# Kernel optimization log

Measured on AMD Instinct MI355X. Metric: run time of the kernel, lower is better.

## Reference

```python
import jax, jax.numpy as jnp
import numpy as np

EPS_NORM = 1e-10
EPS_EXP = 1e-6


def setup_inputs() -> dict:
    key = jax.random.key(0)
    k1, k2 = jax.random.split(key)
    B, F, H, W = 16, 2048, 8, 8
    X = jax.random.normal(k1, (B, F, H, W), dtype=jnp.float32)
    M = jax.random.normal(k2, (B, F, H, W), dtype=jnp.float32)
    return {"X": X, "M": M}


def reference(X, M):
    B, F, H, W = X.shape
    N = H * W
    X = X.reshape(B, F, N)
    M = M.reshape(B, F, N)

    # feature centering over dim=-2 (the feature axis of (B, F, N))
    X = X - X.mean(axis=1, keepdims=True)
    M = M - M.mean(axis=1, keepdims=True)

    # feature_normalize: L2 norm over dim 1, keepdim, + eps
    X = X / (jnp.linalg.norm(X, axis=1, keepdims=True) + EPS_NORM)
    M = M / (jnp.linalg.norm(M, axis=1, keepdims=True) + EPS_NORM)

    # MatmulTopkLoss: S = X @ M^T over spatial N -> (B, F, F)
    S = jnp.einsum('bfn,bgn->bfg', X, M)
    YX = S + jnp.transpose(S, (0, 2, 1))  # symmetrize
    P = jax.nn.softmax(YX, axis=-1)

    k = F // 2
    value, idx = jax.lax.top_k(P, k)  # (B, F, k) values desc, indices
    value_sum = value.sum(axis=-1, keepdims=True)
    row_pos = jnp.arange(F)[None, :, None]  # (1, F, 1)
    dist = jnp.abs(idx - row_pos).astype(value.dtype)
    C_xy = (value * dist / value_sum).mean(axis=-1)  # (B, F)

    xy = jnp.exp(-C_xy + C_xy.min() - EPS_EXP)
    return jnp.reshape(xy.mean(), (1,))
```

## Files before the change

### kernel.cpp

```cpp
#include <hip/hip_runtime.h>
#include <hip/hip_bf16.h>
#include <math.h>

#define B_   16
#define F_   2048
#define N_   64
#define K_   1024
#define YP   2056

typedef short bf16x8 __attribute__((ext_vector_type(8)));
typedef float v4f    __attribute__((ext_vector_type(4)));

__device__ __forceinline__ float wave_sum(float v) {
#pragma unroll
  for (int off = 32; off > 0; off >>= 1) v += __shfl_down(v, off, 64);
  return v;
}
__device__ __forceinline__ float wave_max(float v) {
#pragma unroll
  for (int off = 32; off > 0; off >>= 1) v = fmaxf(v, __shfl_down(v, off, 64));
  return v;
}

__device__ __forceinline__ unsigned f2bf(float x) {
  const unsigned u = __float_as_uint(x);
  return (u + 0x7FFFu + ((u >> 16) & 1u)) >> 16;
}
__device__ __forceinline__ float bf2f(unsigned us) {
  return __uint_as_float(us << 16);
}
__device__ __forceinline__ unsigned ord2u16(unsigned T) {
  return (T & 0x8000u) ? (T ^ 0x8000u) : (T ^ 0xFFFFu);
}

__global__ __launch_bounds__(256) void stats_kernel(
    const float* __restrict__ X, const float* __restrict__ M,
    float* __restrict__ gstats) {
  const int tid = threadIdx.x;
  const int b = blockIdx.x >> 4;
  const int f0 = (blockIdx.x & 15) * 128;
  const int fi = tid >> 6, n = tid & 63;
  float sx = 0.f, sxx = 0.f, sm = 0.f, smm = 0.f;
#pragma unroll 4
  for (int j = 0; j < 32; ++j) {
    const int f = f0 + fi + 4 * j;
    const size_t gi = ((size_t)b * F_ + f) * N_ + n;
    const float x = X[gi];
    const float m = M[gi];
    sx += x; sxx += x * x; sm += m; smm += m * m;
  }
  float* g = gstats + ((size_t)b * N_ + n) * 4;
  atomicAdd(&g[0], sx);
  atomicAdd(&g[1], sxx);
  atomicAdd(&g[2], sm);
  atomicAdd(&g[3], smm);
}

__global__ __launch_bounds__(256) void normbf_kernel(
    const float* __restrict__ X, const float* __restrict__ M,
    const float* __restrict__ gstats,
    short* __restrict__ Xb16, short* __restrict__ Mb16) {
  const int tid = threadIdx.x;
  const int b = blockIdx.x >> 4;
  const int f0 = (blockIdx.x & 15) * 128;
  const int n = tid & 63;
  const float* g = gstats + ((size_t)b * N_ + n) * 4;
  const float sx = g[0], sxx = g[1], sm = g[2], smm = g[3];
  const float mux = sx * (1.f / F_), mum = sm * (1.f / F_);
  const float rx = 1.f / (sqrtf(fmaxf(sxx - (float)F_ * mux * mux, 0.f)) + 1e-10f);
  const float rm = 1.f / (sqrtf(fmaxf(smm - (float)F_ * mum * mum, 0.f)) + 1e-10f);
#pragma unroll 4
  for (int jj = 0; jj < 32; ++jj) {
    const int f = f0 + (tid >> 6) + 4 * jj;
    const size_t gi = ((size_t)b * F_ + f) * N_ + n;
    Xb16[gi] = (short)f2bf((X[gi] - mux) * rx);
    Mb16[gi] = (short)f2bf((M[gi] - mum) * rm);
  }
}

__global__ __launch_bounds__(512)
__attribute__((amdgpu_waves_per_eu(4, 4)))
void rows_kernel(
    const short* __restrict__ Xb16, const short* __restrict__ Mb16,
    float* __restrict__ C) {
  __shared__ unsigned short yxu[16 * YP];
  __shared__ unsigned histS[8 * 256];

  const int tid = threadIdx.x;
  const int w = tid >> 6, lane = tid & 63;
  const int nl = lane & 15, q = lane >> 4;
  const int b = blockIdx.x >> 7;
  const int f0 = (blockIdx.x & 127) * 16;
  const int g0 = 256 * w;

  const short* __restrict__ Xb = Xb16 + (size_t)b * F_ * N_;
  const short* __restrict__ Mb = Mb16 + (size_t)b * F_ * N_;

  const short* Ax = Xb + (size_t)(f0 + nl) * N_ + 8 * q;
  const short* Am = Mb + (size_t)(f0 + nl) * N_ + 8 * q;
  const bf16x8 ax0 = *(const bf16x8*)(Ax);
  const bf16x8 ax1 = *(const bf16x8*)(Ax + 32);
  const bf16x8 am0 = *(const bf16x8*)(Am);
  const bf16x8 am1 = *(const bf16x8*)(Am + 32);

  v4f acc[16];
#pragma unroll
  for (int t = 0; t < 16; ++t) acc[t] = (v4f)(0.f);

#pragma unroll
  for (int t = 0; t < 16; ++t) {
    const short* Bm = Mb + (size_t)(g0 + 16 * t + nl) * N_ + 8 * q;
    const short* Bx = Xb + (size_t)(g0 + 16 * t + nl) * N_ + 8 * q;
    const bf16x8 bm0 = *(const bf16x8*)(Bm);
    const bf16x8 bm1 = *(const bf16x8*)(Bm + 32);
    const bf16x8 bx0 = *(const bf16x8*)(Bx);
    const bf16x8 bx1 = *(const bf16x8*)(Bx + 32);
    acc[t] = __builtin_amdgcn_mfma_f32_16x16x32_bf16(ax0, bm0, acc[t], 0, 0, 0);
    acc[t] = __builtin_amdgcn_mfma_f32_16x16x32_bf16(ax1, bm1, acc[t], 0, 0, 0);
    acc[t] = __builtin_amdgcn_mfma_f32_16x16x32_bf16(am0, bx0, acc[t], 0, 0, 0);
    acc[t] = __builtin_amdgcn_mfma_f32_16x16x32_bf16(am1, bx1, acc[t], 0, 0, 0);
  }

#pragma unroll
  for (int t = 0; t < 16; ++t) {
    const int col = g0 + 16 * t + nl;
#pragma unroll
    for (int r = 0; r < 4; ++r)
      yxu[(4 * q + r) * YP + col] = (unsigned short)f2bf(acc[t][r]);
  }
  __syncthreads();

  unsigned* wh = &histS[w << 8];
#pragma unroll 1
  for (int r4 = 0; r4 < 2; ++r4) {
    const int row = 2 * w + r4;
    const int frow = f0 + row;
    const uint4* rp = (const uint4*)(yxu + row * YP);

    unsigned pk[16];
    unsigned kmin = 0xFFFFFFFFu, kmax = 0u;
#pragma unroll
    for (int j = 0; j < 4; ++j) {
      const uint4 tt = rp[lane + 64 * j];
      const unsigned wds[4] = {tt.x, tt.y, tt.z, tt.w};
#pragma unroll
      for (int c = 0; c < 4; ++c) {
        const unsigned wd = wds[c];
        const unsigned s = wd & 0x80008000u;
        const unsigned o = wd ^ (0x80008000u | ((s >> 15) * 0x7FFFu));
        pk[4 * j + c] = o;
        const unsigned o0 = o & 0xFFFFu, o1 = o >> 16;
        kmin = min(kmin, min(o0, o1));
        kmax = max(kmax, max(o0, o1));
      }
    }
#pragma unroll
    for (int off = 32; off > 0; off >>= 1) {
      kmin = min(kmin, (unsigned)__shfl_down((int)kmin, off, 64));
      kmax = max(kmax, (unsigned)__shfl_down((int)kmax, off, 64));
    }
    kmin = (unsigned)__shfl((int)kmin, 0, 64);
    kmax = (unsigned)__shfl((int)kmax, 0, 64);

    unsigned lo = kmin, R = kmax - kmin, krem = K_;
    unsigned T, tie_need;
    if (R == 0) {
      T = lo; tie_need = krem;
    } else {
      for (;;) {
        const int pos = 31 - __builtin_clz(R);
        const int sh = (pos > 7) ? (pos - 7) : 0;
#pragma unroll
        for (int i = 0; i < 4; ++i) wh[lane + 64 * i] = 0u;
        __builtin_amdgcn_wave_barrier();
#pragma unroll
        for (int c = 0; c < 16; ++c) {
          const unsigned o = pk[c];
          const unsigned d0 = (o & 0xFFFFu) - lo;
          const unsigned d1 = (o >> 16) - lo;
          if (d0 <= R) atomicAdd(&wh[d0 >> sh], 1u);
          if (d1 <= R) atomicAdd(&wh[d1 >> sh], 1u);
        }
        __builtin_amdgcn_wave_barrier();
        unsigned h[4];
#pragma unroll
        for (int i = 0; i < 4; ++i) h[i] = wh[4 * lane + i];
        unsigned s3 = h[3], s2 = h[2] + s3, s1 = h[1] + s2, s0 = h[0] + s1;
        unsigned tot = s0;
#pragma unroll
        for (int off = 1; off < 64; off <<= 1) {
          const unsigned v = __shfl_down(tot, off, 64);
          if (lane + off < 64) tot += v;
        }
        const unsigned above = tot - s0;
        const unsigned S[4] = {above + s0, above + s1, above + s2, above + s3};
        unsigned packed = 0;
        bool found = false;
#pragma unroll
        for (int i = 0; i < 4; ++i) {
          const unsigned Sip1 = S[i] - h[i];
          if (S[i] >= krem && Sip1 < krem) {
            packed = ((unsigned)(4 * lane + i) << 16) | Sip1;
            found = true;
          }
        }
        const unsigned long long bm = __ballot(found);
        const int winner = __ffsll(bm) - 1;
        packed = (unsigned)__shfl((int)packed, winner, 64);
        const unsigned D = packed >> 16;
        krem -= (packed & 0xFFFFu);
        if (sh == 0) { T = lo + D; tie_need = krem; break; }
        lo += (D << sh);
        R = (1u << sh) - 1u;
      }
    }

    float vs = 0.f, ws = 0.f;
    unsigned cnt[4];
#pragma unroll
    for (int j = 0; j < 4; ++j) {
      cnt[j] = 0;
#pragma unroll
      for (int c = 0; c < 4; ++c) {
        const unsigned o = pk[4 * j + c];
        const unsigned oo[2] = {o & 0xFFFFu, o >> 16};
#pragma unroll
        for (int i = 0; i < 2; ++i) {
          const int g = 512 * j + 8 * lane + 2 * c + i;
          if (oo[i] > T) {
            const float pv = __expf(bf2f(ord2u16(oo[i])));
            vs += pv; ws += pv * fabsf((float)(g - frow));
          } else if (oo[i] == T) cnt[j]++;
        }
      }
    }
    const float ptie = __expf(bf2f(ord2u16(T)));

    unsigned pA = cnt[0] | (cnt[1] << 16), pB = cnt[2] | (cnt[3] << 16);
    unsigned iA = pA, iB = pB;
#pragma unroll
    for (int off = 1; off < 64; off <<= 1) {
      const unsigned vA = __shfl_up(iA, off, 64);
      const unsigned vB = __shfl_up(iB, off, 64);
      if (lane >= off) { iA += vA; iB += vB; }
    }
    const unsigned eA = iA - pA, eB = iB - pB;
    const unsigned tA = (unsigned)__shfl((int)iA, 63, 64);
    const unsigned tB = (unsigned)__shfl((int)iB, 63, 64);
    unsigned G[4];
    G[0] = 0;
    G[1] = G[0] + (tA & 0xFFFFu);
    G[2] = G[1] + (tA >> 16);
    G[3] = G[2] + (tB & 0xFFFFu);
#pragma unroll
    for (int j = 0; j < 4; ++j) {
      if (cnt[j]) {
        const unsigned off = (j < 2) ? ((eA >> (16 * j)) & 0xFFFFu)
                                     : ((eB >> (16 * (j - 2))) & 0xFFFFu);
        unsigned cc = 0;
#pragma unroll
        for (int c = 0; c < 4; ++c) {
          const unsigned o = pk[4 * j + c];
          const unsigned oo[2] = {o & 0xFFFFu, o >> 16};
#pragma unroll
          for (int i = 0; i < 2; ++i) {
            if (oo[i] == T) {
              if (G[j] + off + cc < tie_need) {
                const int g = 512 * j + 8 * lane + 2 * c + i;
                vs += ptie; ws += ptie * fabsf((float)(g - frow));
              }
              cc++;
            }
          }
        }
      }
    }

    vs = wave_sum(vs); ws = wave_sum(ws);
    if (lane == 0)
      C[(size_t)b * F_ + frow] = (ws / vs) * (1.f / (float)K_);
  }
}

__global__ __launch_bounds__(1024) void final_kernel(
    const float* __restrict__ C, unsigned* __restrict__ out) {
  __shared__ float red[16];
  const int tid = threadIdx.x;
  const int wave = tid >> 6, lane = tid & 63;
  float v[32];
  float mn = 3.4e38f;
#pragma unroll
  for (int i = 0; i < 32; ++i) {
    v[i] = C[tid + 1024 * i];
    mn = fminf(mn, v[i]);
  }
  mn = -wave_max(-mn);
  if (lane == 0) red[wave] = mn;
  __syncthreads();
  float cmin = red[0];
  for (int w = 1; w < 16; ++w) cmin = fminf(cmin, red[w]);
  __syncthreads();
  float s = 0.f;
#pragma unroll
  for (int i = 0; i < 32; ++i) s += expf(cmin - v[i] - 1e-6f);
  s = wave_sum(s);
  if (lane == 0) red[wave] = s;
  __syncthreads();
  if (tid == 0) {
    float tot = 0.f;
    for (int w = 0; w < 16; ++w) tot += red[w];
    const float res = tot * (1.f / 32768.f);
    const __hip_bfloat16 hb = __float2bfloat16(res);
    const unsigned short u = *(const unsigned short*)&hb;
    out[0] = ((unsigned)u << 16) | (unsigned)u;
  }
}

extern "C" void kernel_launch(void* const* d_in, const int* in_sizes, int n_in,
                              void* d_out, int out_size, void* d_ws, size_t ws_size,
                              hipStream_t stream) {
  const float* X = (const float*)d_in[0];
  const float* M = (const float*)d_in[1];
  short* Xb16 = (short*)d_ws;
  short* Mb16 = Xb16 + (size_t)B_ * F_ * N_;
  float* C = (float*)(Mb16 + (size_t)B_ * F_ * N_);
  float* gstats = C + (size_t)B_ * F_;

  hipMemsetAsync(gstats, 0, (size_t)B_ * N_ * 4 * sizeof(float), stream);
  stats_kernel<<<dim3(B_ * 16), dim3(256), 0, stream>>>(X, M, gstats);
  normbf_kernel<<<dim3(B_ * 16), dim3(256), 0, stream>>>(X, M, gstats, Xb16, Mb16);
  rows_kernel<<<dim3(B_ * (F_ / 16)), dim3(512), 0, stream>>>(Xb16, Mb16, C);
  final_kernel<<<dim3(1), dim3(1024), 0, stream>>>(C, (unsigned*)d_out);
}
```

Before: 235.0 us.

## Process two rows per wave jointly in top-k selection; widen stats grids

The row selection loop now handles both rows of a wave at once. It packs their two histograms into the low and high 16-bit halves of one shared histogram and runs a fixed two-pass radix refinement instead of a data-dependent loop. This interleaves independent work to hide LDS-atomic and shuffle latency, and it halves the histogram clear/scan overhead. The stats and normalize kernels use four times as many blocks with fewer iterations each, to raise occupancy. The fixed two passes assume the 16-bit key range resolves within two 8-bit refinements, and register pressure grows from holding both rows' keys.

```diff
diff --git a/kernel.cpp b/kernel.cpp
--- a/kernel.cpp
+++ b/kernel.cpp
@@ -32,17 +32,20 @@
 __device__ __forceinline__ unsigned ord2u16(unsigned T) {
   return (T & 0x8000u) ? (T ^ 0x8000u) : (T ^ 0xFFFFu);
 }
+__device__ __forceinline__ unsigned ordpair(unsigned wd) {
+  return wd ^ (0x80008000u | (((wd & 0x80008000u) >> 15) * 0x7FFFu));
+}
 
 __global__ __launch_bounds__(256) void stats_kernel(
     const float* __restrict__ X, const float* __restrict__ M,
     float* __restrict__ gstats) {
   const int tid = threadIdx.x;
-  const int b = blockIdx.x >> 4;
-  const int f0 = (blockIdx.x & 15) * 128;
+  const int b = blockIdx.x >> 6;
+  const int f0 = (blockIdx.x & 63) * 32;
   const int fi = tid >> 6, n = tid & 63;
   float sx = 0.f, sxx = 0.f, sm = 0.f, smm = 0.f;
-#pragma unroll 4
-  for (int j = 0; j < 32; ++j) {
+#pragma unroll
+  for (int j = 0; j < 8; ++j) {
     const int f = f0 + fi + 4 * j;
     const size_t gi = ((size_t)b * F_ + f) * N_ + n;
     const float x = X[gi];
@@ -61,16 +64,16 @@
     const float* __restrict__ gstats,
     short* __restrict__ Xb16, short* __restrict__ Mb16) {
   const int tid = threadIdx.x;
-  const int b = blockIdx.x >> 4;
-  const int f0 = (blockIdx.x & 15) * 128;
+  const int b = blockIdx.x >> 6;
+  const int f0 = (blockIdx.x & 63) * 32;
   const int n = tid & 63;
   const float* g = gstats + ((size_t)b * N_ + n) * 4;
   const float sx = g[0], sxx = g[1], sm = g[2], smm = g[3];
   const float mux = sx * (1.f / F_), mum = sm * (1.f / F_);
   const float rx = 1.f / (sqrtf(fmaxf(sxx - (float)F_ * mux * mux, 0.f)) + 1e-10f);
   const float rm = 1.f / (sqrtf(fmaxf(smm - (float)F_ * mum * mum, 0.f)) + 1e-10f);
-#pragma unroll 4
-  for (int jj = 0; jj < 32; ++jj) {
+#pragma unroll
+  for (int jj = 0; jj < 8; ++jj) {
     const int f = f0 + (tid >> 6) + 4 * jj;
     const size_t gi = ((size_t)b * F_ + f) * N_ + n;
     Xb16[gi] = (short)f2bf((X[gi] - mux) * rx);
@@ -131,154 +134,209 @@
   __syncthreads();
 
   unsigned* wh = &histS[w << 8];
-#pragma unroll 1
-  for (int r4 = 0; r4 < 2; ++r4) {
-    const int row = 2 * w + r4;
-    const int frow = f0 + row;
-    const uint4* rp = (const uint4*)(yxu + row * YP);
-
-    unsigned pk[16];
-    unsigned kmin = 0xFFFFFFFFu, kmax = 0u;
-#pragma unroll
-    for (int j = 0; j < 4; ++j) {
-      const uint4 tt = rp[lane + 64 * j];
-      const unsigned wds[4] = {tt.x, tt.y, tt.z, tt.w};
+  const int frow0 = f0 + 2 * w, frow1 = f0 + 2 * w + 1;
+  const uint4* rp0 = (const uint4*)(yxu + (2 * w) * YP);
+  const uint4* rp1 = (const uint4*)(yxu + (2 * w + 1) * YP);
+
+  unsigned pk0[16], pk1[16];
+  unsigned kmin0 = 0xFFFFFFFFu, kmax0 = 0u, kmin1 = 0xFFFFFFFFu, kmax1 = 0u;
+#pragma unroll
+  for (int j = 0; j < 4; ++j) {
+    const uint4 t0 = rp0[lane + 64 * j];
+    const uint4 t1 = rp1[lane + 64 * j];
+    const unsigned w0[4] = {t0.x, t0.y, t0.z, t0.w};
+    const unsigned w1[4] = {t1.x, t1.y, t1.z, t1.w};
+#pragma unroll
+    for (int c = 0; c < 4; ++c) {
+      const unsigned oa = ordpair(w0[c]);
+      pk0[4 * j + c] = oa;
+      kmin0 = min(kmin0, min(oa & 0xFFFFu, oa >> 16));
+      kmax0 = max(kmax0, max(oa & 0xFFFFu, oa >> 16));
+      const unsigned ob = ordpair(w1[c]);
+      pk1[4 * j + c] = ob;
+      kmin1 = min(kmin1, min(ob & 0xFFFFu, ob >> 16));
+      kmax1 = max(kmax1, max(ob & 0xFFFFu, ob >> 16));
+    }
+  }
+#pragma unroll
+  for (int off = 32; off > 0; off >>= 1) {
+    kmin0 = min(kmin0, (unsigned)__shfl_down((int)kmin0, off, 64));
+    kmax0 = max(kmax0, (unsigned)__shfl_down((int)kmax0, off, 64));
+    kmin1 = min(kmin1, (unsigned)__shfl_down((int)kmin1, off, 64));
+    kmax1 = max(kmax1, (unsigned)__shfl_down((int)kmax1, off, 64));
+  }
+  kmin0 = (unsigned)__shfl((int)kmin0, 0, 64);
+  kmax0 = (unsigned)__shfl((int)kmax0, 0, 64);
+  kmin1 = (unsigned)__shfl((int)kmin1, 0, 64);
+  kmax1 = (unsigned)__shfl((int)kmax1, 0, 64);
+
+  unsigned lo0 = kmin0, R0 = kmax0 - kmin0, krem0 = K_, T0 = 0, tie0 = 0;
+  unsigned lo1 = kmin1, R1 = kmax1 - kmin1, krem1 = K_, T1 = 0, tie1 = 0;
+
+#pragma unroll
+  for (int pass = 0; pass < 2; ++pass) {
+    const int pos0 = 31 - __builtin_clz(R0 | 1u);
+    const int sh0 = (pos0 > 7) ? (pos0 - 7) : 0;
+    const int pos1 = 31 - __builtin_clz(R1 | 1u);
+    const int sh1 = (pos1 > 7) ? (pos1 - 7) : 0;
+#pragma unroll
+    for (int i = 0; i < 4; ++i) wh[lane + 64 * i] = 0u;
+    __builtin_amdgcn_wave_barrier();
+#pragma unroll
+    for (int c = 0; c < 16; ++c) {
+      const unsigned oa = pk0[c];
+      const unsigned a0 = (oa & 0xFFFFu) - lo0, a1 = (oa >> 16) - lo0;
+      if (a0 <= R0) atomicAdd(&wh[a0 >> sh0], 1u);
+      if (a1 <= R0) atomicAdd(&wh[a1 >> sh0], 1u);
+      const unsigned ob = pk1[c];
+      const unsigned b0 = (ob & 0xFFFFu) - lo1, b1 = (ob >> 16) - lo1;
+      if (b0 <= R1) atomicAdd(&wh[b0 >> sh1], 0x10000u);
+      if (b1 <= R1) atomicAdd(&wh[b1 >> sh1], 0x10000u);
+    }
+    __builtin_amdgcn_wave_barrier();
+    unsigned h[4];
+#pragma unroll
+    for (int i = 0; i < 4; ++i) h[i] = wh[4 * lane + i];
+    const unsigned s3 = h[3], s2 = h[2] + s3, s1 = h[1] + s2, s0 = h[0] + s1;
+    unsigned tot = s0;
+#pragma unroll
+    for (int off = 1; off < 64; off <<= 1) {
+      const unsigned v = __shfl_down(tot, off, 64);
+      if (lane + off < 64) tot += v;
+    }
+    const unsigned above = tot - s0;
+    const unsigned S[4] = {above + s0, above + s1, above + s2, above + s3};
+    unsigned p0 = 0, p1 = 0;
+    bool fb0 = false, fb1 = false;
+#pragma unroll
+    for (int i = 0; i < 4; ++i) {
+      const unsigned Sl = S[i] & 0xFFFFu, hl = h[i] & 0xFFFFu;
+      const unsigned Spl = Sl - hl;
+      if (Sl >= krem0 && Spl < krem0) {
+        p0 = ((unsigned)(4 * lane + i) << 16) | Spl; fb0 = true;
+      }
+      const unsigned Sh = S[i] >> 16, hh = h[i] >> 16;
+      const unsigned Sph = Sh - hh;
+      if (Sh >= krem1 && Sph < krem1) {
+        p1 = ((unsigned)(4 * lane + i) << 16) | Sph; fb1 = true;
+      }
+    }
+    const int wi0 = __ffsll(__ballot(fb0)) - 1;
+    const int wi1 = __ffsll(__ballot(fb1)) - 1;
+    p0 = (unsigned)__shfl((int)p0, wi0, 64);
+    p1 = (unsigned)__shfl((int)p1, wi1, 64);
+    const unsigned D0 = p0 >> 16, D1 = p1 >> 16;
+    krem0 -= (p0 & 0xFFFFu);
+    krem1 -= (p1 & 0xFFFFu);
+    if (sh0 == 0) { T0 = lo0 + D0; tie0 = krem0; lo0 = T0; R0 = 0; }
+    else          { lo0 += (D0 << sh0); R0 = (1u << sh0) - 1u; }
+    if (sh1 == 0) { T1 = lo1 + D1; tie1 = krem1; lo1 = T1; R1 = 0; }
+    else          { lo1 += (D1 << sh1); R1 = (1u << sh1) - 1u; }
+  }
+
+  float vs0 = 0.f, ws0 = 0.f, vs1 = 0.f, ws1 = 0.f;
+  unsigned cnt0[4], cnt1[4];
+#pragma unroll
+  for (int j = 0; j < 4; ++j) {
+    cnt0[j] = 0; cnt1[j] = 0;
+#pragma unroll
+    for (int c = 0; c < 4; ++c) {
+      const unsigned oa = pk0[4 * j + c];
+      const unsigned aa[2] = {oa & 0xFFFFu, oa >> 16};
+      const unsigned ob = pk1[4 * j + c];
+      const unsigned bb[2] = {ob & 0xFFFFu, ob >> 16};
+#pragma unroll
+      for (int i = 0; i < 2; ++i) {
+        const int g = 512 * j + 8 * lane + 2 * c + i;
+        if (aa[i] > T0) {
+          const float pv = __expf(bf2f(ord2u16(aa[i])));
+          vs0 += pv; ws0 += pv * fabsf((float)(g - frow0));
+        } else if (aa[i] == T0) cnt0[j]++;
+        if (bb[i] > T1) {
+          const float pv = __expf(bf2f(ord2u16(bb[i])));
+          vs1 += pv; ws1 += pv * fabsf((float)(g - frow1));
+        } else if (bb[i] == T1) cnt1[j]++;
+      }
+    }
+  }
+  const float pt0 = __expf(bf2f(ord2u16(T0)));
+  const float pt1 = __expf(bf2f(ord2u16(T1)));
+
+  unsigned pA0 = cnt0[0] | (cnt0[1] << 16), pB0 = cnt0[2] | (cnt0[3] << 16);
+  unsigned pA1 = cnt1[0] | (cnt1[1] << 16), pB1 = cnt1[2] | (cnt1[3] << 16);
+  unsigned iA0 = pA0, iB0 = pB0, iA1 = pA1, iB1 = pB1;
+#pragma unroll
+  for (int off = 1; off < 64; off <<= 1) {
+    const unsigned vA0 = __shfl_up(iA0, off, 64);
+    const unsigned vB0 = __shfl_up(iB0, off, 64);
+    const unsigned vA1 = __shfl_up(iA1, off, 64);
+    const unsigned vB1 = __shfl_up(iB1, off, 64);
+    if (lane >= off) { iA0 += vA0; iB0 += vB0; iA1 += vA1; iB1 += vB1; }
+  }
+  const unsigned eA0 = iA0 - pA0, eB0 = iB0 - pB0;
+  const unsigned eA1 = iA1 - pA1, eB1 = iB1 - pB1;
+  const unsigned tA0 = (unsigned)__shfl((int)iA0, 63, 64);
+  const unsigned tB0 = (unsigned)__shfl((int)iB0, 63, 64);
+  const unsigned tA1 = (unsigned)__shfl((int)iA1, 63, 64);
+  const unsigned tB1 = (unsigned)__shfl((int)iB1, 63, 64);
+  unsigned G0[4], G1[4];
+  G0[0] = 0;
+  G0[1] = G0[0] + (tA0 & 0xFFFFu);
+  G0[2] = G0[1] + (tA0 >> 16);
+  G0[3] = G0[2] + (tB0 & 0xFFFFu);
+  G1[0] = 0;
+  G1[1] = G1[0] + (tA1 & 0xFFFFu);
+  G1[2] = G1[1] + (tA1 >> 16);
+  G1[3] = G1[2] + (tB1 & 0xFFFFu);
+#pragma unroll
+  for (int j = 0; j < 4; ++j) {
+    if (cnt0[j]) {
+      const unsigned off = (j < 2) ? ((eA0 >> (16 * j)) & 0xFFFFu)
+                                   : ((eB0 >> (16 * (j - 2))) & 0xFFFFu);
+      unsigned cc = 0;
 #pragma unroll
       for (int c = 0; c < 4; ++c) {
-        const unsigned wd = wds[c];
-        const unsigned s = wd & 0x80008000u;
-        const unsigned o = wd ^ (0x80008000u | ((s >> 15) * 0x7FFFu));
-        pk[4 * j + c] = o;
-        const unsigned o0 = o & 0xFFFFu, o1 = o >> 16;
-        kmin = min(kmin, min(o0, o1));
-        kmax = max(kmax, max(o0, o1));
-      }
-    }
-#pragma unroll
-    for (int off = 32; off > 0; off >>= 1) {
-      kmin = min(kmin, (unsigned)__shfl_down((int)kmin, off, 64));
-      kmax = max(kmax, (unsigned)__shfl_down((int)kmax, off, 64));
-    }
-    kmin = (unsigned)__shfl((int)kmin, 0, 64);
-    kmax = (unsigned)__shfl((int)kmax, 0, 64);
-
-    unsigned lo = kmin, R = kmax - kmin, krem = K_;
-    unsigned T, tie_need;
-    if (R == 0) {
-      T = lo; tie_need = krem;
-    } else {
-      for (;;) {
-        const int pos = 31 - __builtin_clz(R);
-        const int sh = (pos > 7) ? (pos - 7) : 0;
-#pragma unroll
-        for (int i = 0; i < 4; ++i) wh[lane + 64 * i] = 0u;
-        __builtin_amdgcn_wave_barrier();
-#pragma unroll
-        for (int c = 0; c < 16; ++c) {
-          const unsigned o = pk[c];
-          const unsigned d0 = (o & 0xFFFFu) - lo;
-          const unsigned d1 = (o >> 16) - lo;
-          if (d0 <= R) atomicAdd(&wh[d0 >> sh], 1u);
-          if (d1 <= R) atomicAdd(&wh[d1 >> sh], 1u);
-        }
-        __builtin_amdgcn_wave_barrier();
-        unsigned h[4];
-#pragma unroll
-        for (int i = 0; i < 4; ++i) h[i] = wh[4 * lane + i];
-        unsigned s3 = h[3], s2 = h[2] + s3, s1 = h[1] + s2, s0 = h[0] + s1;
-        unsigned tot = s0;
-#pragma unroll
-        for (int off = 1; off < 64; off <<= 1) {
-          const unsigned v = __shfl_down(tot, off, 64);
-          if (lane + off < 64) tot += v;
-        }
-        const unsigned above = tot - s0;
-        const unsigned S[4] = {above + s0, above + s1, above + s2, above + s3};
-        unsigned packed = 0;
-        bool found = false;
-#pragma unroll
-        for (int i = 0; i < 4; ++i) {
-          const unsigned Sip1 = S[i] - h[i];
-          if (S[i] >= krem && Sip1 < krem) {
-            packed = ((unsigned)(4 * lane + i) << 16) | Sip1;
-            found = true;
+        const unsigned o = pk0[4 * j + c];
+        const unsigned oo[2] = {o & 0xFFFFu, o >> 16};
+#pragma unroll
+        for (int i = 0; i < 2; ++i) {
+          if (oo[i] == T0) {
+            if (G0[j] + off + cc < tie0) {
+              const int g = 512 * j + 8 * lane + 2 * c + i;
+              vs0 += pt0; ws0 += pt0 * fabsf((float)(g - frow0));
+            }
+            cc++;
           }
         }
-        const unsigned long long bm = __ballot(found);
-        const int winner = __ffsll(bm) - 1;
-        packed = (unsigned)__shfl((int)packed, winner, 64);
-        const unsigned D = packed >> 16;
-        krem -= (packed & 0xFFFFu);
-        if (sh == 0) { T = lo + D; tie_need = krem; break; }
-        lo += (D << sh);
-        R = (1u << sh) - 1u;
-      }
-    }
-
-    float vs = 0.f, ws = 0.f;
-    unsigned cnt[4];
-#pragma unroll
-    for (int j = 0; j < 4; ++j) {
-      cnt[j] = 0;
+      }
+    }
+    if (cnt1[j]) {
+      const unsigned off = (j < 2) ? ((eA1 >> (16 * j)) & 0xFFFFu)
+                                   : ((eB1 >> (16 * (j - 2))) & 0xFFFFu);
+      unsigned cc = 0;
 #pragma unroll
       for (int c = 0; c < 4; ++c) {
-        const unsigned o = pk[4 * j + c];
+        const unsigned o = pk1[4 * j + c];
         const unsigned oo[2] = {o & 0xFFFFu, o >> 16};
 #pragma unroll
         for (int i = 0; i < 2; ++i) {
-          const int g = 512 * j + 8 * lane + 2 * c + i;
-          if (oo[i] > T) {
-            const float pv = __expf(bf2f(ord2u16(oo[i])));
-            vs += pv; ws += pv * fabsf((float)(g - frow));
-          } else if (oo[i] == T) cnt[j]++;
-        }
-      }
-    }
-    const float ptie = __expf(bf2f(ord2u16(T)));
-
-    unsigned pA = cnt[0] | (cnt[1] << 16), pB = cnt[2] | (cnt[3] << 16);
-    unsigned iA = pA, iB = pB;
-#pragma unroll
-    for (int off = 1; off < 64; off <<= 1) {
-      const unsigned vA = __shfl_up(iA, off, 64);
-      const unsigned vB = __shfl_up(iB, off, 64);
-      if (lane >= off) { iA += vA; iB += vB; }
-    }
-    const unsigned eA = iA - pA, eB = iB - pB;
-    const unsigned tA = (unsigned)__shfl((int)iA, 63, 64);
-    const unsigned tB = (unsigned)__shfl((int)iB, 63, 64);
-    unsigned G[4];
-    G[0] = 0;
-    G[1] = G[0] + (tA & 0xFFFFu);
-    G[2] = G[1] + (tA >> 16);
-    G[3] = G[2] + (tB & 0xFFFFu);
-#pragma unroll
-    for (int j = 0; j < 4; ++j) {
-      if (cnt[j]) {
-        const unsigned off = (j < 2) ? ((eA >> (16 * j)) & 0xFFFFu)
-                                     : ((eB >> (16 * (j - 2))) & 0xFFFFu);
-        unsigned cc = 0;
-#pragma unroll
-        for (int c = 0; c < 4; ++c) {
-          const unsigned o = pk[4 * j + c];
-          const unsigned oo[2] = {o & 0xFFFFu, o >> 16};
-#pragma unroll
-          for (int i = 0; i < 2; ++i) {
-            if (oo[i] == T) {
-              if (G[j] + off + cc < tie_need) {
-                const int g = 512 * j + 8 * lane + 2 * c + i;
-                vs += ptie; ws += ptie * fabsf((float)(g - frow));
-              }
-              cc++;
+          if (oo[i] == T1) {
+            if (G1[j] + off + cc < tie1) {
+              const int g = 512 * j + 8 * lane + 2 * c + i;
+              vs1 += pt1; ws1 += pt1 * fabsf((float)(g - frow1));
             }
+            cc++;
           }
         }
       }
     }
-
-    vs = wave_sum(vs); ws = wave_sum(ws);
-    if (lane == 0)
-      C[(size_t)b * F_ + frow] = (ws / vs) * (1.f / (float)K_);
+  }
+
+  vs0 = wave_sum(vs0); ws0 = wave_sum(ws0);
+  vs1 = wave_sum(vs1); ws1 = wave_sum(ws1);
+  if (lane == 0) {
+    C[(size_t)b * F_ + frow0] = (ws0 / vs0) * (1.f / (float)K_);
+    C[(size_t)b * F_ + frow1] = (ws1 / vs1) * (1.f / (float)K_);
   }
 }
 
@@ -327,8 +385,8 @@
   float* gstats = C + (size_t)B_ * F_;
 
   hipMemsetAsync(gstats, 0, (size_t)B_ * N_ * 4 * sizeof(float), stream);
-  stats_kernel<<<dim3(B_ * 16), dim3(256), 0, stream>>>(X, M, gstats);
-  normbf_kernel<<<dim3(B_ * 16), dim3(256), 0, stream>>>(X, M, gstats, Xb16, Mb16);
+  stats_kernel<<<dim3(B_ * 64), dim3(256), 0, stream>>>(X, M, gstats);
+  normbf_kernel<<<dim3(B_ * 64), dim3(256), 0, stream>>>(X, M, gstats, Xb16, Mb16);
   rows_kernel<<<dim3(B_ * (F_ / 16)), dim3(512), 0, stream>>>(Xb16, Mb16, C);
   final_kernel<<<dim3(1), dim3(1024), 0, stream>>>(C, (unsigned*)d_out);
 }
```

New measurement: 272.3 us. 1.16x slower.
